# Kernel optimization log

Hardware: AMD Instinct MI355X
Metric: run time of the kernel (lower is better)

Reference implementation:

```python
import jax, jax.numpy as jnp
import numpy as np


def setup_inputs() -> dict:
    key = jax.random.key(0)
    k1, k2, k3 = jax.random.split(key, 3)
    B, T, Din, D = 32, 2048, 256, 256
    x = jax.random.normal(k1, (B, T, Din), dtype=jnp.float32)
    # glorot-ish scaling for stability
    W = jax.random.normal(k2, (Din, 4 * D), dtype=jnp.float32) * (1.0 / np.sqrt(Din))
    U = jax.random.normal(k3, (D, 4 * D), dtype=jnp.float32) * (1.0 / np.sqrt(D))
    b = jnp.zeros((4 * D,), dtype=jnp.float32)
    return {"x": x, "W": W, "U": U, "b": b}


def reference(x, W, U, b):
    # x: [B, T, Din]; W: [Din, 4D]; U: [D, 4D]; b: [4D]
    # Gate slice order (per original step()): 0=i, 1=f, 2=o, 3=candidate
    D = U.shape[0]
    B = x.shape[0]
    # Precompute input projections for all timesteps in one big matmul.
    px = jnp.einsum('btd,df->tbf', x, W) + b  # [T, B, 4D]

    def step(carry, px_t):
        h, c = carry
        preact = px_t + h @ U  # [B, 4D]
        i = jax.nn.sigmoid(preact[:, 0 * D:1 * D])
        f = jax.nn.sigmoid(preact[:, 1 * D:2 * D])
        o = jax.nn.sigmoid(preact[:, 2 * D:3 * D])
        g = jnp.tanh(preact[:, 3 * D:4 * D])
        c_new = f * c + i * g
        h_new = o * jnp.tanh(c_new)
        return (h_new, c_new), h_new

    h0 = jnp.zeros((B, D), dtype=x.dtype)
    c0 = jnp.zeros((B, D), dtype=x.dtype)
    _, h_seq = jax.lax.scan(step, (h0, c0), px)  # h_seq: [T, B, D]
    return jnp.transpose(h_seq, (1, 0, 2))  # output_sequence: [B, T, D]
```

## Files before the change

kernel.cpp:

```cpp
#include <hip/hip_runtime.h>
#include <math.h>

#define B_SZ 32
#define T_SZ 2048
#define DIN 256
#define DH 256
#define FOUR_D 1024

#define NW 8
#define DPW 32

#define IK16(k) ((k) + ((k) >> 6) * 8)
#define USTR 264

typedef _Float16 f16x2 __attribute__((ext_vector_type(2)));

#if __has_builtin(__builtin_amdgcn_fdot2)
#define FDOT2(a, b, c) __builtin_amdgcn_fdot2((a), (b), (c), false)
#else
__device__ __forceinline__ float fdot2_emu(f16x2 a, f16x2 b, float c) {
    return c + (float)a[0] * (float)b[0] + (float)a[1] * (float)b[1];
}
#define FDOT2(a, b, c) fdot2_emu((a), (b), (c))
#endif

__device__ __forceinline__ f16x2 H2(float f) {
    union { float f; f16x2 h; } u; u.f = f; return u.h;
}

__global__ void zero_ws(unsigned int* p, int n) {
    int i = blockIdx.x * blockDim.x + threadIdx.x;
    if (i < n) p[i] = 0u;
}

__global__ __launch_bounds__(256) void px_gemm(
    const float* __restrict__ x, const float* __restrict__ W,
    const float* __restrict__ bias, float* __restrict__ px,
    int t0)
{
    __shared__ float xt[16][DIN];
    const int tid = threadIdx.x;
    const int rbase = blockIdx.x * 16;

    {
        int row = tid >> 4;
        int seg = (tid & 15) * 16;
        int r = rbase + row;
        int bb = r & 31;
        int tt = r >> 5;
        const float4* s4 = (const float4*)(x + ((size_t)bb * T_SZ + (size_t)(t0 + tt)) * DIN + seg);
        float4* dst = (float4*)&xt[row][seg];
        dst[0] = s4[0]; dst[1] = s4[1]; dst[2] = s4[2]; dst[3] = s4[3];
    }
    __syncthreads();

    const int j = tid * 4;
    float4 bv = *(const float4*)&bias[j];
    float acc[16][4];
#pragma unroll
    for (int r = 0; r < 16; ++r) {
        acc[r][0] = bv.x; acc[r][1] = bv.y; acc[r][2] = bv.z; acc[r][3] = bv.w;
    }

    for (int k = 0; k < DIN; k += 4) {
        float4 w0 = *(const float4*)&W[(size_t)(k + 0) * FOUR_D + j];
        float4 w1 = *(const float4*)&W[(size_t)(k + 1) * FOUR_D + j];
        float4 w2 = *(const float4*)&W[(size_t)(k + 2) * FOUR_D + j];
        float4 w3 = *(const float4*)&W[(size_t)(k + 3) * FOUR_D + j];
#pragma unroll
        for (int r = 0; r < 16; ++r) {
            float4 xv = *(const float4*)&xt[r][k];
            acc[r][0] += xv.x * w0.x + xv.y * w1.x + xv.z * w2.x + xv.w * w3.x;
            acc[r][1] += xv.x * w0.y + xv.y * w1.y + xv.z * w2.y + xv.w * w3.y;
            acc[r][2] += xv.x * w0.z + xv.y * w1.z + xv.z * w2.z + xv.w * w3.z;
            acc[r][3] += xv.x * w0.w + xv.y * w1.w + xv.z * w2.w + xv.w * w3.w;
        }
    }

#pragma unroll
    for (int r = 0; r < 16; ++r) {
        float4 st = make_float4(acc[r][0], acc[r][1], acc[r][2], acc[r][3]);
        *(float4*)&px[((size_t)(rbase + r)) * FOUR_D + j] = st;
    }
}

__global__ __launch_bounds__(512, 2) void lstm_scan15(
    const float* __restrict__ px, const float* __restrict__ U,
    float* __restrict__ out, unsigned long long* __restrict__ hbuf,
    float* __restrict__ cstate, int t0, int ct)
{
    __shared__ _Float16 u_lds[128 * USTR];
    __shared__ _Float16 h1_lds[2][288];

    const int b = blockIdx.x >> 3;
    const int w = blockIdx.x & 7;
    const int tid = threadIdx.x;
    const int dd = tid >> 4;
    const int gate = (tid >> 2) & 3;
    const int seg = tid & 3;
    const int colg = (gate << 8) + (w << 5) + dd;
    const int d = (w << 5) + dd;
    const bool pub = (tid & 15) == 0;

    for (int it = 0; it < 64; ++it) {
        int lin = (it << 9) + tid;
        int row = lin & 127;
        int kk = lin >> 7;
        int gcol = ((row & 3) << 8) + (w << 5) + (row >> 2);
        float v = U[(size_t)kk * FOUR_D + gcol];
        int sg = kk >> 6;
        int cc = (kk >> 3) & 7;
        int jj = kk & 7;
        int p = ((cc >> 1) << 3) + (sg << 1) + (cc & 1);
        u_lds[row * USTR + (p << 3) + jj] = (_Float16)v;
    }
    float c_reg = cstate[b * DH + d];
    __syncthreads();

    const int rowbase = (dd * 4 + gate) * USTR;
    float4 uq[8];
#pragma unroll
    for (int c2 = 0; c2 < 8; ++c2) {
        int p = ((c2 >> 1) << 3) + (seg << 1) + (c2 & 1);
        uq[c2] = *(const float4*)&u_lds[rowbase + (p << 3)];
    }
#pragma unroll
    for (int c2 = 0; c2 < 8; ++c2) {
        asm volatile("" : "+v"(uq[c2].x), "+v"(uq[c2].y),
                          "+v"(uq[c2].z), "+v"(uq[c2].w));
    }

    for (int tt = 0; tt < ct; ++tt) {
        const int s = t0 + tt + 1;

        float pxv = px[((size_t)tt * B_SZ + b) * FOUR_D + colg];

        if (tid < DH) {
            const bool local = (tid >> 5) == w;
            if (tt == 0 && t0 == 0) {
                h1_lds[0][IK16(tid)] = (_Float16)0.0f;
            } else if (tt == 0 || !local) {
                const unsigned long long want = (unsigned long long)(unsigned)(s - 1);
                const unsigned long long* slot = hbuf +
                    (((size_t)((s - 1) & 1) * B_SZ + b) * DH + tid);
                unsigned long long v;
                do {
                    v = __hip_atomic_load(slot, __ATOMIC_RELAXED,
                                          __HIP_MEMORY_SCOPE_AGENT);
                } while ((v >> 32) != want);
                h1_lds[tt & 1][IK16(tid)] = (_Float16)__uint_as_float((unsigned)v);
            }
        }
        __syncthreads();

        const _Float16* hrow = &h1_lds[tt & 1][seg * 72];
        float a0 = 0.f, a1 = 0.f, a2 = 0.f, a3 = 0.f;
#pragma unroll
        for (int c2 = 0; c2 < 8; ++c2) {
            float4 hv = *(const float4*)&hrow[c2 << 3];
            a0 = FDOT2(H2(uq[c2].x), H2(hv.x), a0);
            a1 = FDOT2(H2(uq[c2].y), H2(hv.y), a1);
            a2 = FDOT2(H2(uq[c2].z), H2(hv.z), a2);
            a3 = FDOT2(H2(uq[c2].w), H2(hv.w), a3);
        }
        float pr = (a0 + a1) + (a2 + a3);

        pr += __shfl_xor(pr, 1);
        pr += __shfl_xor(pr, 2);
        float pre = pxv + pr;

        float act;
        if (gate < 3) {
            act = 1.0f / (1.0f + __expf(-pre));
        } else {
            float e = __expf(-2.0f * pre);
            act = 2.0f / (1.0f + e) - 1.0f;
        }

        const int bl = (tid & 48) | seg;
        float ig = __shfl(act, bl);
        float fg = __shfl(act, bl | 4);
        float og = __shfl(act, bl | 8);
        float gv = __shfl(act, bl | 12);

        float cn = fg * c_reg + ig * gv;
        c_reg = cn;
        float ec = __expf(-2.0f * cn);
        float hn = og * (2.0f / (1.0f + ec) - 1.0f);

        if (pub) {
            unsigned long long pv =
                ((unsigned long long)(unsigned)s << 32) |
                (unsigned long long)__float_as_uint(hn);
            __hip_atomic_store(hbuf + (((size_t)(s & 1) * B_SZ + b) * DH + d),
                               pv, __ATOMIC_RELAXED, __HIP_MEMORY_SCOPE_AGENT);
            h1_lds[(tt + 1) & 1][IK16(d)] = (_Float16)hn;
            out[((size_t)b * T_SZ + (size_t)(s - 1)) * DH + d] = hn;
        }
    }

    if (pub) cstate[b * DH + d] = c_reg;
}

extern "C" void kernel_launch(void* const* d_in, const int* in_sizes, int n_in,
                              void* d_out, int out_size, void* d_ws, size_t ws_size,
                              hipStream_t stream) {
    const float* x    = (const float*)d_in[0];
    const float* W    = (const float*)d_in[1];
    const float* U    = (const float*)d_in[2];
    const float* bias = (const float*)d_in[3];
    float* out = (float*)d_out;

    float* cstate = (float*)d_ws;
    unsigned long long* hbuf = (unsigned long long*)((char*)d_ws + 32 * 1024);
    size_t px_off = 160 * 1024;
    float* pxbuf = (float*)((char*)d_ws + px_off);

    size_t avail = (ws_size > px_off) ? (ws_size - px_off) : 0;
    size_t per_step = (size_t)B_SZ * FOUR_D * sizeof(float);
    long ct_max = (long)(avail / per_step);
    int CT = (ct_max >= T_SZ) ? T_SZ : (int)ct_max;
    if (CT < 1) CT = 1;

    int zero_words = (160 * 1024) / 4;
    zero_ws<<<(zero_words + 255) / 256, 256, 0, stream>>>((unsigned int*)d_ws, zero_words);

    for (int t0 = 0; t0 < T_SZ; t0 += CT) {
        int ct = (T_SZ - t0 < CT) ? (T_SZ - t0) : CT;
        int rows = ct * B_SZ;
        px_gemm<<<rows / 16, 256, 0, stream>>>(x, W, bias, pxbuf, t0);
        lstm_scan15<<<B_SZ * NW, 512, 0, stream>>>(pxbuf, U, out, hbuf, cstate, t0, ct);
    }
}
```

Baseline: 3.457 ms.

## Pack two fp16 hidden values per flag slot and poll with 16-byte loads

The cross-block hidden-state exchange now publishes two fp16 h values per 64-bit tagged slot, halving the slot count, and readers poll with one 16-byte cache-bypassing load that fetches four h values at once. Only 64 threads poll instead of 256, which cuts the number of polling memory transactions per timestep on the serial recurrent path. A fallback to per-slot atomic loads after repeated misses handles cases where the wide load sees the two halves torn. The cost is inline assembly with cache-control bits specific to this target, plus an extra shuffle to pair neighbouring h values.

```diff
diff --git a/kernel.cpp b/kernel.cpp
--- a/kernel.cpp
+++ b/kernel.cpp
@@ -9,6 +9,7 @@
 
 #define NW 8
 #define DPW 32
+#define NSLOT 128
 
 #define IK16(k) ((k) + ((k) >> 6) * 8)
 #define USTR 264
@@ -26,6 +27,9 @@
 
 __device__ __forceinline__ f16x2 H2(float f) {
     union { float f; f16x2 h; } u; u.f = f; return u.h;
+}
+__device__ __forceinline__ unsigned short F16B(float f) {
+    union { _Float16 h; unsigned short u; } cu; cu.h = (_Float16)f; return cu.u;
 }
 
 __global__ void zero_ws(unsigned int* p, int n) {
@@ -84,7 +88,15 @@
     }
 }
 
-__global__ __launch_bounds__(512, 2) void lstm_scan15(
+__device__ __forceinline__ uint4 poll_load16(const unsigned long long* p) {
+    uint4 r;
+    asm volatile("global_load_dwordx4 %0, %1, off sc0 sc1\n\t"
+                 "s_waitcnt vmcnt(0)"
+                 : "=v"(r) : "v"(p) : "memory");
+    return r;
+}
+
+__global__ __launch_bounds__(512, 2) void lstm_scan16(
     const float* __restrict__ px, const float* __restrict__ U,
     float* __restrict__ out, unsigned long long* __restrict__ hbuf,
     float* __restrict__ cstate, int t0, int ct)
@@ -135,20 +147,36 @@
 
         float pxv = px[((size_t)tt * B_SZ + b) * FOUR_D + colg];
 
-        if (tid < DH) {
-            const bool local = (tid >> 5) == w;
+        if (tid < 64) {
+            const bool local = (tid >> 3) == w;
             if (tt == 0 && t0 == 0) {
-                h1_lds[0][IK16(tid)] = (_Float16)0.0f;
+                *(unsigned long long*)&h1_lds[0][IK16(tid << 2)] = 0ull;
             } else if (tt == 0 || !local) {
-                const unsigned long long want = (unsigned long long)(unsigned)(s - 1);
-                const unsigned long long* slot = hbuf +
-                    (((size_t)((s - 1) & 1) * B_SZ + b) * DH + tid);
-                unsigned long long v;
-                do {
-                    v = __hip_atomic_load(slot, __ATOMIC_RELAXED,
-                                          __HIP_MEMORY_SCOPE_AGENT);
-                } while ((v >> 32) != want);
-                h1_lds[tt & 1][IK16(tid)] = (_Float16)__uint_as_float((unsigned)v);
+                const unsigned want = (unsigned)(s - 1);
+                const unsigned long long* slotp = hbuf +
+                    ((size_t)((s - 1) & 1) * B_SZ + b) * NSLOT + (tid << 1);
+                unsigned long long hh;
+                int tries = 0;
+                for (;;) {
+                    uint4 v = poll_load16(slotp);
+                    if (v.y == want && v.w == want) {
+                        hh = (unsigned long long)v.x |
+                             ((unsigned long long)v.z << 32);
+                        break;
+                    }
+                    if (++tries > 64) {
+                        unsigned long long q0, q1;
+                        do { q0 = __hip_atomic_load(slotp, __ATOMIC_RELAXED,
+                                                    __HIP_MEMORY_SCOPE_AGENT);
+                        } while ((unsigned)(q0 >> 32) != want);
+                        do { q1 = __hip_atomic_load(slotp + 1, __ATOMIC_RELAXED,
+                                                    __HIP_MEMORY_SCOPE_AGENT);
+                        } while ((unsigned)(q1 >> 32) != want);
+                        hh = (q0 & 0xffffffffull) | (q1 << 32);
+                        break;
+                    }
+                }
+                *(unsigned long long*)&h1_lds[tt & 1][IK16(tid << 2)] = hh;
             }
         }
         __syncthreads();
@@ -188,12 +216,17 @@
         float ec = __expf(-2.0f * cn);
         float hn = og * (2.0f / (1.0f + ec) - 1.0f);
 
+        float hn_n = __shfl_xor(hn, 16);
+
         if (pub) {
-            unsigned long long pv =
-                ((unsigned long long)(unsigned)s << 32) |
-                (unsigned long long)__float_as_uint(hn);
-            __hip_atomic_store(hbuf + (((size_t)(s & 1) * B_SZ + b) * DH + d),
-                               pv, __ATOMIC_RELAXED, __HIP_MEMORY_SCOPE_AGENT);
+            if ((dd & 1) == 0) {
+                unsigned long long pv =
+                    ((unsigned long long)(unsigned)s << 32) |
+                    ((unsigned)F16B(hn_n) << 16) | (unsigned)F16B(hn);
+                __hip_atomic_store(
+                    hbuf + ((size_t)(s & 1) * B_SZ + b) * NSLOT + (d >> 1),
+                    pv, __ATOMIC_RELAXED, __HIP_MEMORY_SCOPE_AGENT);
+            }
             h1_lds[(tt + 1) & 1][IK16(d)] = (_Float16)hn;
             out[((size_t)b * T_SZ + (size_t)(s - 1)) * DH + d] = hn;
         }
@@ -229,6 +262,6 @@
         int ct = (T_SZ - t0 < CT) ? (T_SZ - t0) : CT;
         int rows = ct * B_SZ;
         px_gemm<<<rows / 16, 256, 0, stream>>>(x, W, bias, pxbuf, t0);
-        lstm_scan15<<<B_SZ * NW, 512, 0, stream>>>(pxbuf, U, out, hbuf, cstate, t0, ct);
-    }
-}
+        lstm_scan16<<<B_SZ * NW, 512, 0, stream>>>(pxbuf, U, out, hbuf, cstate, t0, ct);
+    }
+}
```

Measured after the change: 3.724 ms. 1.08x slower.

## Fuse input projection into recurrent LSTM scan kernel with fp16 W in LDS

Applied to the files above, without the earlier changes.

Drops the separate px GEMM and the px workspace buffer. Each scan block now keeps an fp16 copy of its slice of W in LDS and computes the input projection x_t·W per step inside the recurrence, prefetching x one step ahead. This removes the global round trip for px and the chunked launch loop. The cost is more LDS (lower occupancy headroom), extra per-step dot-product work on the serial critical path, and input projection now done in fp16.

```diff
diff --git a/kernel.cpp b/kernel.cpp
--- a/kernel.cpp
+++ b/kernel.cpp
@@ -33,64 +33,15 @@
     if (i < n) p[i] = 0u;
 }
 
-__global__ __launch_bounds__(256) void px_gemm(
+__global__ __launch_bounds__(512, 2) void lstm_fused4(
     const float* __restrict__ x, const float* __restrict__ W,
-    const float* __restrict__ bias, float* __restrict__ px,
-    int t0)
-{
-    __shared__ float xt[16][DIN];
-    const int tid = threadIdx.x;
-    const int rbase = blockIdx.x * 16;
-
-    {
-        int row = tid >> 4;
-        int seg = (tid & 15) * 16;
-        int r = rbase + row;
-        int bb = r & 31;
-        int tt = r >> 5;
-        const float4* s4 = (const float4*)(x + ((size_t)bb * T_SZ + (size_t)(t0 + tt)) * DIN + seg);
-        float4* dst = (float4*)&xt[row][seg];
-        dst[0] = s4[0]; dst[1] = s4[1]; dst[2] = s4[2]; dst[3] = s4[3];
-    }
-    __syncthreads();
-
-    const int j = tid * 4;
-    float4 bv = *(const float4*)&bias[j];
-    float acc[16][4];
-#pragma unroll
-    for (int r = 0; r < 16; ++r) {
-        acc[r][0] = bv.x; acc[r][1] = bv.y; acc[r][2] = bv.z; acc[r][3] = bv.w;
-    }
-
-    for (int k = 0; k < DIN; k += 4) {
-        float4 w0 = *(const float4*)&W[(size_t)(k + 0) * FOUR_D + j];
-        float4 w1 = *(const float4*)&W[(size_t)(k + 1) * FOUR_D + j];
-        float4 w2 = *(const float4*)&W[(size_t)(k + 2) * FOUR_D + j];
-        float4 w3 = *(const float4*)&W[(size_t)(k + 3) * FOUR_D + j];
-#pragma unroll
-        for (int r = 0; r < 16; ++r) {
-            float4 xv = *(const float4*)&xt[r][k];
-            acc[r][0] += xv.x * w0.x + xv.y * w1.x + xv.z * w2.x + xv.w * w3.x;
-            acc[r][1] += xv.x * w0.y + xv.y * w1.y + xv.z * w2.y + xv.w * w3.y;
-            acc[r][2] += xv.x * w0.z + xv.y * w1.z + xv.z * w2.z + xv.w * w3.z;
-            acc[r][3] += xv.x * w0.w + xv.y * w1.w + xv.z * w2.w + xv.w * w3.w;
-        }
-    }
-
-#pragma unroll
-    for (int r = 0; r < 16; ++r) {
-        float4 st = make_float4(acc[r][0], acc[r][1], acc[r][2], acc[r][3]);
-        *(float4*)&px[((size_t)(rbase + r)) * FOUR_D + j] = st;
-    }
-}
-
-__global__ __launch_bounds__(512, 2) void lstm_scan15(
-    const float* __restrict__ px, const float* __restrict__ U,
-    float* __restrict__ out, unsigned long long* __restrict__ hbuf,
-    float* __restrict__ cstate, int t0, int ct)
+    const float* __restrict__ U, const float* __restrict__ bias,
+    float* __restrict__ out, unsigned long long* __restrict__ hbuf)
 {
     __shared__ _Float16 u_lds[128 * USTR];
+    __shared__ _Float16 w_lds[128 * USTR];
     __shared__ _Float16 h1_lds[2][288];
+    __shared__ _Float16 x_lds[2][288];
 
     const int b = blockIdx.x >> 3;
     const int w = blockIdx.x & 7;
@@ -107,22 +58,32 @@
         int row = lin & 127;
         int kk = lin >> 7;
         int gcol = ((row & 3) << 8) + (w << 5) + (row >> 2);
-        float v = U[(size_t)kk * FOUR_D + gcol];
         int sg = kk >> 6;
         int cc = (kk >> 3) & 7;
         int jj = kk & 7;
         int p = ((cc >> 1) << 3) + (sg << 1) + (cc & 1);
-        u_lds[row * USTR + (p << 3) + jj] = (_Float16)v;
+        int idx = row * USTR + (p << 3) + jj;
+        u_lds[idx] = (_Float16)U[(size_t)kk * FOUR_D + gcol];
+        w_lds[idx] = (_Float16)W[(size_t)kk * FOUR_D + gcol];
     }
-    float c_reg = cstate[b * DH + d];
+    float4 xr = make_float4(0.f, 0.f, 0.f, 0.f);
+    if (tid < 64) {
+        float4 v0 = *(const float4*)&x[((size_t)b * T_SZ) * DIN + tid * 4];
+        _Float16* dst = &x_lds[0][IK16(tid * 4)];
+        dst[0] = (_Float16)v0.x; dst[1] = (_Float16)v0.y;
+        dst[2] = (_Float16)v0.z; dst[3] = (_Float16)v0.w;
+        xr = *(const float4*)&x[((size_t)b * T_SZ + 1) * DIN + tid * 4];
+    }
+    const float binit = (seg == 0) ? bias[colg] : 0.0f;
+    float c_reg = 0.0f;
     __syncthreads();
 
-    const int rowbase = (dd * 4 + gate) * USTR;
+    const int rowb = (dd * 4 + gate) * USTR;
     float4 uq[8];
 #pragma unroll
     for (int c2 = 0; c2 < 8; ++c2) {
         int p = ((c2 >> 1) << 3) + (seg << 1) + (c2 & 1);
-        uq[c2] = *(const float4*)&u_lds[rowbase + (p << 3)];
+        uq[c2] = *(const float4*)&u_lds[rowb + (p << 3)];
     }
 #pragma unroll
     for (int c2 = 0; c2 < 8; ++c2) {
@@ -130,19 +91,38 @@
                           "+v"(uq[c2].z), "+v"(uq[c2].w));
     }
 
-    for (int tt = 0; tt < ct; ++tt) {
-        const int s = t0 + tt + 1;
+    for (int tt = 0; tt < T_SZ; ++tt) {
+        if (tid < 64) {
+            if (tt + 1 < T_SZ) {
+                _Float16* dst = &x_lds[(tt + 1) & 1][IK16(tid * 4)];
+                dst[0] = (_Float16)xr.x; dst[1] = (_Float16)xr.y;
+                dst[2] = (_Float16)xr.z; dst[3] = (_Float16)xr.w;
+            }
+            if (tt + 2 < T_SZ)
+                xr = *(const float4*)&x[((size_t)b * T_SZ + tt + 2) * DIN + tid * 4];
+        }
 
-        float pxv = px[((size_t)tt * B_SZ + b) * FOUR_D + colg];
+        const _Float16* xrow = &x_lds[tt & 1][seg * 72];
+        float a0 = binit, a1 = 0.f, a2 = 0.f, a3 = 0.f;
+#pragma unroll
+        for (int c2 = 0; c2 < 8; ++c2) {
+            int p = ((c2 >> 1) << 3) + (seg << 1) + (c2 & 1);
+            float4 wv = *(const float4*)&w_lds[rowb + (p << 3)];
+            float4 xv = *(const float4*)&xrow[c2 << 3];
+            a0 = FDOT2(H2(wv.x), H2(xv.x), a0);
+            a1 = FDOT2(H2(wv.y), H2(xv.y), a1);
+            a2 = FDOT2(H2(wv.z), H2(xv.z), a2);
+            a3 = FDOT2(H2(wv.w), H2(xv.w), a3);
+        }
 
         if (tid < DH) {
             const bool local = (tid >> 5) == w;
-            if (tt == 0 && t0 == 0) {
+            if (tt == 0) {
                 h1_lds[0][IK16(tid)] = (_Float16)0.0f;
-            } else if (tt == 0 || !local) {
-                const unsigned long long want = (unsigned long long)(unsigned)(s - 1);
+            } else if (!local) {
+                const unsigned long long want = (unsigned long long)(unsigned)tt;
                 const unsigned long long* slot = hbuf +
-                    (((size_t)((s - 1) & 1) * B_SZ + b) * DH + tid);
+                    (((size_t)(tt & 1) * B_SZ + b) * DH + tid);
                 unsigned long long v;
                 do {
                     v = __hip_atomic_load(slot, __ATOMIC_RELAXED,
@@ -154,7 +134,6 @@
         __syncthreads();
 
         const _Float16* hrow = &h1_lds[tt & 1][seg * 72];
-        float a0 = 0.f, a1 = 0.f, a2 = 0.f, a3 = 0.f;
 #pragma unroll
         for (int c2 = 0; c2 < 8; ++c2) {
             float4 hv = *(const float4*)&hrow[c2 << 3];
@@ -167,7 +146,7 @@
 
         pr += __shfl_xor(pr, 1);
         pr += __shfl_xor(pr, 2);
-        float pre = pxv + pr;
+        float pre = pr;
 
         float act;
         if (gate < 3) {
@@ -190,16 +169,14 @@
 
         if (pub) {
             unsigned long long pv =
-                ((unsigned long long)(unsigned)s << 32) |
+                ((unsigned long long)(unsigned)(tt + 1) << 32) |
                 (unsigned long long)__float_as_uint(hn);
-            __hip_atomic_store(hbuf + (((size_t)(s & 1) * B_SZ + b) * DH + d),
+            __hip_atomic_store(hbuf + (((size_t)((tt + 1) & 1) * B_SZ + b) * DH + d),
                                pv, __ATOMIC_RELAXED, __HIP_MEMORY_SCOPE_AGENT);
             h1_lds[(tt + 1) & 1][IK16(d)] = (_Float16)hn;
-            out[((size_t)b * T_SZ + (size_t)(s - 1)) * DH + d] = hn;
+            out[((size_t)b * T_SZ + tt) * DH + d] = hn;
         }
     }
-
-    if (pub) cstate[b * DH + d] = c_reg;
 }
 
 extern "C" void kernel_launch(void* const* d_in, const int* in_sizes, int n_in,
@@ -211,24 +188,10 @@
     const float* bias = (const float*)d_in[3];
     float* out = (float*)d_out;
 
-    float* cstate = (float*)d_ws;
-    unsigned long long* hbuf = (unsigned long long*)((char*)d_ws + 32 * 1024);
-    size_t px_off = 160 * 1024;
-    float* pxbuf = (float*)((char*)d_ws + px_off);
+    unsigned long long* hbuf = (unsigned long long*)d_ws;
 
-    size_t avail = (ws_size > px_off) ? (ws_size - px_off) : 0;
-    size_t per_step = (size_t)B_SZ * FOUR_D * sizeof(float);
-    long ct_max = (long)(avail / per_step);
-    int CT = (ct_max >= T_SZ) ? T_SZ : (int)ct_max;
-    if (CT < 1) CT = 1;
-
-    int zero_words = (160 * 1024) / 4;
+    int zero_words = (128 * 1024) / 4;
     zero_ws<<<(zero_words + 255) / 256, 256, 0, stream>>>((unsigned int*)d_ws, zero_words);
 
-    for (int t0 = 0; t0 < T_SZ; t0 += CT) {
-        int ct = (T_SZ - t0 < CT) ? (T_SZ - t0) : CT;
-        int rows = ct * B_SZ;
-        px_gemm<<<rows / 16, 256, 0, stream>>>(x, W, bias, pxbuf, t0);
-        lstm_scan15<<<B_SZ * NW, 512, 0, stream>>>(pxbuf, U, out, hbuf, cstate, t0, ct);
-    }
+    lstm_fused4<<<B_SZ * NW, 512, 0, stream>>>(x, W, U, bias, out, hbuf);
 }
```

Result: faster. 2.988 ms (-13.6%).
